# Kernel tuning notes

Measured on AMD Instinct MI355X. Metric: run time of the kernel, lower is better.

The kernel has to match this reference:

```python
import jax, jax.numpy as jnp
import numpy as np

ALPHA = 0.2          # LeakyReLU negative slope
NEG_BIG = -9e15      # mask value from the original code


def setup_inputs() -> dict:
    key = jax.random.key(0)
    k1, k2, k3, k4, k5 = jax.random.split(key, 5)
    N, Fin, Fout, C = 8192, 2048, 256, 8
    x = jax.random.normal(k1, (N, Fin), dtype=jnp.float32)
    # xavier_uniform-ish scale for params
    W = jax.random.normal(k2, (C, Fin, Fout), dtype=jnp.float32) / np.sqrt(Fin).astype(np.float32)
    a = jax.random.normal(k3, (2 * Fout, 1), dtype=jnp.float32) / np.sqrt(2 * Fout).astype(np.float32)
    cam_ids = jax.random.randint(k4, (N,), 0, C, dtype=jnp.int32)
    adj = jax.random.randint(k5, (N, N), 0, 2, dtype=jnp.int32)
    return {"x": x, "W": W, "a": a, "cam_ids": cam_ids, "adj": adj}


def reference(x, W, a, cam_ids, adj):
    N = x.shape[0]
    Fout = W.shape[-1]
    # per-node camera-specific projection: h[i] = x[i] @ W[cam_ids[i]]
    # compute all-camera projections (N, C, Fout) then gather per node;
    # avoids materializing W[cam_ids] of shape (N, Fin, Fout)
    hs = jnp.einsum('nd,cdo->nco', x, W)                       # (N, C, Fout)
    h = jnp.take_along_axis(hs, cam_ids[:, None, None], axis=1)[:, 0, :]  # (N, Fout)
    # e_ij = leakyrelu([h_i, h_j] @ a) = leakyrelu(h_i.a1 + h_j.a2)
    a1 = a[:Fout, 0]
    a2 = a[Fout:, 0]
    e = jax.nn.leaky_relu((h @ a1)[:, None] + (h @ a2)[None, :], ALPHA)  # (N, N)
    att = jnp.where(adj > 0, e, jnp.float32(NEG_BIG))
    att = jax.nn.softmax(att, axis=1)
    # dropout is identity at eval (p applied only in training)
    h_prime = att @ h                                          # (N, Fout)
    return jax.nn.elu(h_prime)                                 # concat=True -> ELU
```

## Files before the change

### kernel.cpp

```cpp
#include <hip/hip_runtime.h>

#define NR 8192
#define FIN 2048
#define FOUT 256
#define ALPHA 0.2f
#define NTMAX 136
#define KS 4
#define KLEN 512
#define NSTEPS 16
#define JC 4
#define NJ 2048

typedef float f32x4 __attribute__((ext_vector_type(4)));
typedef float f32x16 __attribute__((ext_vector_type(16)));
typedef int i32x4 __attribute__((ext_vector_type(4)));
typedef unsigned int u32x4 __attribute__((ext_vector_type(4)));
typedef unsigned short u16x4 __attribute__((ext_vector_type(4)));
typedef unsigned short u16x8 __attribute__((ext_vector_type(8)));
typedef __bf16 bf16x8 __attribute__((ext_vector_type(8)));
typedef _Float16 f16x8 __attribute__((ext_vector_type(8)));

__device__ __forceinline__ unsigned short f2bf(float f){
  unsigned u = __float_as_uint(f);
  return (unsigned short)((u + 0x7fffu + ((u >> 16) & 1u)) >> 16);
}
__device__ __forceinline__ float bf2f(unsigned short b){
  return __uint_as_float(((unsigned)b) << 16);
}
__device__ __forceinline__ void gload16(const void* gptr, void* lptr){
  __builtin_amdgcn_global_load_lds(
      (const __attribute__((address_space(1))) unsigned int*)gptr,
      (__attribute__((address_space(3))) unsigned int*)lptr, 16, 0, 0);
}

#define FBAR() do{ \
  asm volatile("s_waitcnt lgkmcnt(0)" ::: "memory"); \
  __builtin_amdgcn_s_barrier(); \
  __builtin_amdgcn_sched_barrier(0); }while(0)

__global__ __launch_bounds__(256) void k_pre(const float* __restrict__ W,
    _Float16* __restrict__ WhT, const int* __restrict__ cam,
    int* __restrict__ prows, int* __restrict__ tileCam){
  __shared__ __align__(16) char smem[9216];
  int blk = blockIdx.x, t = threadIdx.x;
  if (blk < 1024){
    _Float16 (*tl)[72] = (_Float16(*)[72])smem;
    int k0 = (blk & 31) << 6;
    int n0 = ((blk >> 5) & 3) << 6;
    int c = blk >> 7;
    {
      int kk = t >> 2, nq = (t & 3)*16;
      const float* src = W + ((size_t)c*FIN + k0 + kk)*FOUT + n0 + nq;
      #pragma unroll
      for (int q = 0; q < 4; q++){
        f32x4 v = *(const f32x4*)(src + q*4);
        #pragma unroll
        for (int e = 0; e < 4; e++) tl[nq + q*4 + e][kk] = (_Float16)v[e];
      }
    }
    __syncthreads();
    {
      int nn = t >> 2, kq = (t & 3)*16;
      union { u32x4 v[2]; _Float16 s[16]; } buf;
      #pragma unroll
      for (int e = 0; e < 16; e++) buf.s[e] = tl[nn][kq + e];
      u32x4* dst = (u32x4*)(WhT + ((size_t)c*FOUT + n0 + nn)*FIN + k0 + kq);
      dst[0] = buf.v[0]; dst[1] = buf.v[1];
    }
  } else {
    int (*cnt)[8] = (int(*)[8])smem;
    int* scnt = (int*)(smem + 8192);
    int* tst  = (int*)(smem + 8224);
    int loc[8];
    #pragma unroll
    for (int c = 0; c < 8; c++) loc[c] = 0;
    for (int k = 0; k < 32; k++) loc[cam[t*32 + k] & 7]++;
    #pragma unroll
    for (int c = 0; c < 8; c++) cnt[t][c] = loc[c];
    __syncthreads();
    if (t < 8){
      int s = 0;
      for (int i = 0; i < 256; i++){ int v = cnt[i][t]; cnt[i][t] = s; s += v; }
      scnt[t] = s;
    }
    __syncthreads();
    if (t == 0){
      int ts = 0;
      for (int c = 0; c < 8; c++){ tst[c] = ts; ts += (scnt[c] + 63) >> 6; }
      tst[8] = ts;
    }
    __syncthreads();
    for (int s = t; s < NTMAX*64; s += 256) prows[s] = -1;
    if (t < NTMAX){
      int tc = -1, te = tst[8];
      if (t < te){
        #pragma unroll
        for (int c = 0; c < 8; c++)
          if (t >= tst[c] && t < tst[c+1]) tc = c;
      }
      tileCam[t] = tc;
    }
    __syncthreads();
    int off[8];
    #pragma unroll
    for (int c = 0; c < 8; c++) off[c] = cnt[t][c];
    for (int k = 0; k < 32; k++){
      int n = t*32 + k; int c = cam[n] & 7;
      int slot = off[c]++;
      prows[(tst[c] + (slot >> 6))*64 + (slot & 63)] = n;
    }
  }
}

__global__ __launch_bounds__(256, 3) void k_gmm(const float* __restrict__ x,
    const _Float16* __restrict__ WhT, const int* __restrict__ tileCam,
    const int* __restrict__ prows, float* __restrict__ partial){
  __shared__ __align__(16) char smem[41728];
  int item = blockIdx.x;
  int tile = item >> 2, ks = item & 3;
  int camc = tileCam[tile];
  if (camc < 0) return;
  _Float16* ab = (_Float16*)smem;
  int* rows  = (int*)(smem + 40960);
  int* growL = (int*)(smem + 41216);
  int t = threadIdx.x;
  if (t < 64){
    int r = prows[tile*64 + t];
    rows[t] = r; growL[t] = (r < 0) ? 0 : r;
  }
  __syncthreads();
  int lane = t & 63, w = t >> 6;
  int k0 = ks * KLEN;
  int wr = w >> 1, wc = w & 1;
  int rA = ((t >> 6) & 1)*32 + (t & 31);
  int koffA = (t >> 7)*16 + ((t >> 5) & 1)*8;
  const float* srcA = x + (size_t)growL[rA]*FIN + k0 + koffA;
  const _Float16* srcB[4];
  #pragma unroll
  for (int q = 0; q < 4; q++){
    int c2 = q*256 + t;
    int colg = ((c2 >> 6) & 7)*32 + (t & 31);
    srcB[q] = WhT + ((size_t)camc*FOUT + colg)*FIN + k0
            + (c2 >> 9)*16 + ((t >> 5) & 1)*8;
  }
  f32x16 acc[4];
  #pragma unroll
  for (int nb = 0; nb < 4; nb++)
    #pragma unroll
    for (int r = 0; r < 16; r++) acc[nb][r] = 0.f;
  int cur = 0;
  {
    f32x4 a0 = *(const f32x4*)srcA;
    f32x4 a1 = *(const f32x4*)(srcA + 4);
    #pragma unroll
    for (int q = 0; q < 4; q++) gload16(srcB[q], &ab[2048 + (q*256 + t)*8]);
    f16x8 hv;
    #pragma unroll
    for (int e = 0; e < 4; e++){ hv[e] = (_Float16)a0[e]; hv[4+e] = (_Float16)a1[e]; }
    *(f16x8*)&ab[t*8] = hv;
  }
  __syncthreads();
  for (int s = 0; s < NSTEPS; s++){
    bool have = (s + 1 < NSTEPS);
    int adv = have ? (s + 1)*32 : 0;
    f32x4 na0 = *(const f32x4*)(srcA + adv);
    f32x4 na1 = *(const f32x4*)(srcA + adv + 4);
    if (have){
      #pragma unroll
      for (int q = 0; q < 4; q++)
        gload16(srcB[q] + adv, &ab[(cur ^ 1)*10240 + 2048 + (q*256 + t)*8]);
    }
    const _Float16* base = ab + cur*10240;
    f16x8 af[2]; f16x8 bfr[2][4];
    #pragma unroll
    for (int kk = 0; kk < 2; kk++){
      af[kk] = *(const f16x8*)(base + ((kk*2 + wr)*64 + lane)*8);
      #pragma unroll
      for (int nb = 0; nb < 4; nb++)
        bfr[kk][nb] = *(const f16x8*)(base + 2048 + ((kk*8 + wc*4 + nb)*64 + lane)*8);
    }
    #pragma unroll
    for (int kk = 0; kk < 2; kk++)
      #pragma unroll
      for (int nb = 0; nb < 4; nb++)
        acc[nb] = __builtin_amdgcn_mfma_f32_32x32x16_f16(af[kk], bfr[kk][nb], acc[nb], 0, 0, 0);
    if (have){
      f16x8 hv;
      #pragma unroll
      for (int e = 0; e < 4; e++){ hv[e] = (_Float16)na0[e]; hv[4+e] = (_Float16)na1[e]; }
      *(f16x8*)&ab[(cur ^ 1)*10240 + t*8] = hv;
    }
    __syncthreads();
    cur ^= 1;
  }
  int colb = wc*128;
  #pragma unroll
  for (int nb = 0; nb < 4; nb++){
    #pragma unroll
    for (int r = 0; r < 16; r++){
      int rowl = wr*32 + (r & 3) + 8*(r >> 2) + 4*(lane >> 5);
      int grow = rows[rowl];
      if (grow >= 0)
        partial[((size_t)ks*NR + grow)*FOUT + colb + nb*32 + (lane & 31)] = acc[nb][r];
    }
  }
}

__global__ __launch_bounds__(256) void k_hsumT(const float* __restrict__ partial,
    const float* __restrict__ a, float* __restrict__ s1, float* __restrict__ s2,
    float* __restrict__ bm, unsigned short* __restrict__ hT){
  __shared__ __align__(16) char smem[36096];
  unsigned short* sums = (unsigned short*)smem;
  float* a1l = (float*)(smem + 33792);
  float* a2l = (float*)(smem + 34816);
  float* redv = (float*)(smem + 35840);
  int blk = blockIdx.x, t = threadIdx.x;
  int w = t >> 6, lane = t & 63;
  int r0 = blk*64;
  a1l[t] = a[t]; a2l[t] = a[FOUT + t];
  __syncthreads();
  float bmax = -3.0e38f;
  #pragma unroll
  for (int rep = 0; rep < 16; rep++){
    int row = rep*4 + w;
    const float* pp = partial + (size_t)(r0 + row)*FOUT + lane*4;
    f32x4 s; s[0] = s[1] = s[2] = s[3] = 0.f;
    #pragma unroll
    for (int ks = 0; ks < KS; ks++)
      s += *(const f32x4*)(pp + (size_t)ks*NR*FOUT);
    u16x4 pk;
    #pragma unroll
    for (int e = 0; e < 4; e++) pk[e] = f2bf(s[e]);
    *(u16x4*)&sums[row*264 + lane*4] = pk;
    f32x4 a1v = *(const f32x4*)&a1l[lane*4];
    f32x4 a2v = *(const f32x4*)&a2l[lane*4];
    float p1 = 0.f, p2 = 0.f;
    #pragma unroll
    for (int e = 0; e < 4; e++){ p1 = fmaf(s[e], a1v[e], p1); p2 = fmaf(s[e], a2v[e], p2); }
    #pragma unroll
    for (int off2 = 32; off2 > 0; off2 >>= 1){
      p1 += __shfl_xor(p1, off2);
      p2 += __shfl_xor(p2, off2);
    }
    if (lane == 0){
      s1[r0 + row] = p1; s2[r0 + row] = p2;
      bmax = fmaxf(bmax, p2);
    }
  }
  if (lane == 0) redv[w] = bmax;
  __syncthreads();
  if (t == 0)
    bm[blk] = fmaxf(fmaxf(redv[0], redv[1]), fmaxf(redv[2], redv[3]));
  int c = t;
  #pragma unroll
  for (int q = 0; q < 8; q++){
    u16x8 v;
    #pragma unroll
    for (int e = 0; e < 8; e++) v[e] = sums[(q*8 + e)*264 + c];
    *(u16x8*)(hT + (size_t)c*NR + r0 + q*8) = v;
  }
}

__global__ __launch_bounds__(512, 4) void k_flash(const int* __restrict__ adj,
    const float* __restrict__ s1g, const float* __restrict__ s2g,
    const float* __restrict__ bm, const unsigned short* __restrict__ hT,
    float* __restrict__ hp, float* __restrict__ Dp){
  __shared__ __align__(16) unsigned short hTl[256*64];
  __shared__ __align__(16) unsigned short pl[64][72];
  __shared__ float s1l[64], ml[64], Dl[64], red[8];
  int blk = blockIdx.x, t = threadIdx.x;
  int w = t >> 6, lane = t & 63;
  int it = blk & 127, jc = blk >> 7;
  int i0 = it*64;
  int jbase = jc * NJ;
  {
    float v = (t < 128) ? bm[t] : -3.0e38f;
    #pragma unroll
    for (int off = 32; off > 0; off >>= 1) v = fmaxf(v, __shfl_xor(v, off));
    if (lane == 0) red[w] = v;
  }
  __syncthreads();
  if (t == 0){
    float v = red[0];
    #pragma unroll
    for (int k = 1; k < 8; k++) v = fmaxf(v, red[k]);
    red[0] = v;
  }
  __syncthreads();
  float maxS2 = red[0];
  if (t < 64){
    float sv = s1g[i0 + t];
    s1l[t] = sv;
    float mm = sv + maxS2;
    ml[t] = fmaxf(mm, ALPHA*mm);
  }
  __syncthreads();
  int il = t >> 3, tj = t & 7;
  float s1i = s1l[il], mi = ml[il];
  float Dacc = 0.f;
  f32x16 acc0, acc1;
  #pragma unroll
  for (int k = 0; k < 16; k++){ acc0[k] = 0.f; acc1[k] = 0.f; }
  const unsigned short* hsrc[4];
  int ldst[4];
  #pragma unroll
  for (int q = 0; q < 4; q++){
    int g = t + 512*q;
    int row = g >> 3, part = g & 7;
    hsrc[q] = hT + (size_t)row*NR + jbase + part*8;
    ldst[q] = row*64 + ((part ^ (row & 7))*8);
  }
  const int* arow = adj + (size_t)(i0 + il)*NR + jbase + tj*8;
  i32x4 adx[2][2];
  f32x4 s2x[2][2];
  #pragma unroll
  for (int sl = 0; sl < 2; sl++){
    adx[sl][0] = __builtin_nontemporal_load((const i32x4*)(arow + sl*64));
    adx[sl][1] = __builtin_nontemporal_load((const i32x4*)(arow + sl*64) + 1);
    s2x[sl][0] = *(const f32x4*)(s2g + jbase + sl*64 + tj*8);
    s2x[sl][1] = *(const f32x4*)(s2g + jbase + sl*64 + tj*8 + 4);
  }
  u32x4 hch[4];
  #pragma unroll
  for (int q = 0; q < 4; q++) hch[q] = *(const u32x4*)hsrc[q];
  for (int jt = 0; jt < NJ; jt += 128){
    #pragma unroll
    for (int half = 0; half < 2; half++){
      int jcur = jt + half*64;
      i32x4 c0 = adx[half][0], c1 = adx[half][1];
      f32x4 t0 = s2x[half][0], t1 = s2x[half][1];
      int jn2 = (jcur + 128 < NJ) ? jcur + 128 : 0;
      adx[half][0] = __builtin_nontemporal_load((const i32x4*)(arow + jn2));
      adx[half][1] = __builtin_nontemporal_load((const i32x4*)(arow + jn2) + 1);
      s2x[half][0] = *(const f32x4*)(s2g + jbase + jn2 + tj*8);
      s2x[half][1] = *(const f32x4*)(s2g + jbase + jn2 + tj*8 + 4);
      u16x8 pu;
      float Dloc = 0.f;
      #pragma unroll
      for (int e = 0; e < 4; e++){
        float e0 = s1i + t0[e]; e0 = fmaxf(e0, ALPHA*e0);
        float p0 = (c0[e] > 0) ? __expf(e0 - mi) : 0.f;
        unsigned short b0 = f2bf(p0); pu[e] = b0; Dloc += bf2f(b0);
        float e1 = s1i + t1[e]; e1 = fmaxf(e1, ALPHA*e1);
        float p1 = (c1[e] > 0) ? __expf(e1 - mi) : 0.f;
        unsigned short b1 = f2bf(p1); pu[e + 4] = b1; Dloc += bf2f(b1);
      }
      Dacc += Dloc;
      *(u16x8*)&pl[il][tj*8] = pu;
      #pragma unroll
      for (int q = 0; q < 4; q++) *(u32x4*)&hTl[ldst[q]] = hch[q];
      FBAR();
      int jn1 = (jcur + 64 < NJ) ? jcur + 64 : 0;
      #pragma unroll
      for (int q = 0; q < 4; q++) hch[q] = *(const u32x4*)(hsrc[q] + jn1);
      int nrow = w*32 + (lane & 31);
      #pragma unroll
      for (int ks = 0; ks < 4; ks++){
        int p = ks*2 + (lane >> 5);
        bf16x8 B = *(const bf16x8*)&hTl[nrow*64 + ((p ^ (nrow & 7))*8)];
        int koff = ks*16 + (lane >> 5)*8;
        bf16x8 a0 = *(const bf16x8*)&pl[lane & 31][koff];
        acc0 = __builtin_amdgcn_mfma_f32_32x32x16_bf16(a0, B, acc0, 0, 0, 0);
        bf16x8 a1 = *(const bf16x8*)&pl[32 + (lane & 31)][koff];
        acc1 = __builtin_amdgcn_mfma_f32_32x32x16_bf16(a1, B, acc1, 0, 0, 0);
      }
      FBAR();
    }
  }
  Dacc += __shfl_xor(Dacc, 1);
  Dacc += __shfl_xor(Dacc, 2);
  Dacc += __shfl_xor(Dacc, 4);
  if (tj == 0) Dl[il] = Dacc;
  __syncthreads();
  if (t < 64) Dp[(size_t)jc*NR + i0 + t] = Dl[t];
  float* hpb = hp + (size_t)jc*NR*FOUT;
  int col = w*32 + (lane & 31);
  #pragma unroll
  for (int r = 0; r < 16; r++){
    int rowl = (r & 3) + 8*(r >> 2) + 4*(lane >> 5);
    hpb[(size_t)(i0 + rowl)*FOUT + col] = acc0[r];
    hpb[(size_t)(i0 + 32 + rowl)*FOUT + col] = acc1[r];
  }
}

__global__ __launch_bounds__(256) void k_final(const float* __restrict__ hp,
    const float* __restrict__ Dp, float* __restrict__ out){
  int g = blockIdx.x*256 + threadIdx.x;
  int i = g >> 6, cg4 = (g & 63)*4;
  f32x4 s; s[0] = s[1] = s[2] = s[3] = 0.f;
  float D = 0.f;
  #pragma unroll
  for (int jc = 0; jc < JC; jc++){
    s += *(const f32x4*)(hp + ((size_t)jc*NR + i)*FOUT + cg4);
    D += Dp[(size_t)jc*NR + i];
  }
  float inv = (D > 0.f) ? 1.f / D : 0.f;
  f32x4 o;
  #pragma unroll
  for (int e = 0; e < 4; e++){
    float v = s[e]*inv;
    o[e] = (v > 0.f) ? v : expm1f(v);
  }
  *(f32x4*)(out + (size_t)i*FOUT + cg4) = o;
}

extern "C" void kernel_launch(void* const* d_in, const int* in_sizes, int n_in,
                              void* d_out, int out_size, void* d_ws, size_t ws_size,
                              hipStream_t stream){
  (void)in_sizes; (void)n_in; (void)out_size; (void)ws_size;
  const float* x   = (const float*)d_in[0];
  const float* W   = (const float*)d_in[1];
  const float* a   = (const float*)d_in[2];
  const int*   cam = (const int*)d_in[3];
  const int*   adj = (const int*)d_in[4];
  float* out = (float*)d_out;
  char* ws = (char*)d_ws;

  size_t off = 0;
  auto alloc = [&](size_t b) -> void* {
    void* p = ws + off; off = (off + b + 255) & ~(size_t)255; return p;
  };
  int* tileCam  = (int*)alloc((size_t)NTMAX*4);
  int* prows    = (int*)alloc((size_t)NTMAX*64*4);
  _Float16* WhT = (_Float16*)alloc((size_t)8*FIN*FOUT*2);
  unsigned short* hT = (unsigned short*)alloc((size_t)NR*FOUT*2);
  float* s1 = (float*)alloc((size_t)NR*4);
  float* s2 = (float*)alloc((size_t)NR*4);
  float* bm = (float*)alloc(128*4);
  float* Dp = (float*)alloc((size_t)JC*NR*4);
  float* partial = (float*)alloc((size_t)KS*NR*FOUT*4);
  float* hp = partial;

  hipLaunchKernelGGL(k_pre, dim3(1025), dim3(256), 0, stream,
                     W, WhT, cam, prows, tileCam);
  hipLaunchKernelGGL(k_gmm, dim3(NTMAX*4), dim3(256), 0, stream,
                     x, WhT, tileCam, prows, partial);
  hipLaunchKernelGGL(k_hsumT, dim3(128), dim3(256), 0, stream,
                     partial, a, s1, s2, bm, hT);
  hipLaunchKernelGGL(k_flash, dim3(512), dim3(512), 0, stream,
                     adj, s1, s2, bm, hT, hp, Dp);
  hipLaunchKernelGGL(k_final, dim3((NR*FOUT/4)/256), dim3(256), 0, stream,
                     hp, Dp, out);
}
```

Baseline: 207.3 us.

## Fuse final normalize+ELU into flash kernel via last-block atomic counter

Removes the separate k_final launch. The last of the JC column-chunk blocks for each row tile, detected with an atomic counter, reduces the partial hp/Dp, normalizes and applies ELU directly. It also replaces the custom FBAR barrier (explicit lgkmcnt wait plus sched_barrier) with plain __syncthreads. This saves a launch and some tail latency, but adds fences and atomics and may lose the scheduling control FBAR gave.

```diff
diff --git a/kernel.cpp b/kernel.cpp
--- a/kernel.cpp
+++ b/kernel.cpp
@@ -33,14 +33,10 @@
       (__attribute__((address_space(3))) unsigned int*)lptr, 16, 0, 0);
 }
 
-#define FBAR() do{ \
-  asm volatile("s_waitcnt lgkmcnt(0)" ::: "memory"); \
-  __builtin_amdgcn_s_barrier(); \
-  __builtin_amdgcn_sched_barrier(0); }while(0)
-
 __global__ __launch_bounds__(256) void k_pre(const float* __restrict__ W,
     _Float16* __restrict__ WhT, const int* __restrict__ cam,
-    int* __restrict__ prows, int* __restrict__ tileCam){
+    int* __restrict__ prows, int* __restrict__ tileCam,
+    int* __restrict__ fcnt){
   __shared__ __align__(16) char smem[9216];
   int blk = blockIdx.x, t = threadIdx.x;
   if (blk < 1024){
@@ -68,6 +64,7 @@
       dst[0] = buf.v[0]; dst[1] = buf.v[1];
     }
   } else {
+    if (t < 128) fcnt[t] = 0;
     int (*cnt)[8] = (int(*)[8])smem;
     int* scnt = (int*)(smem + 8192);
     int* tst  = (int*)(smem + 8224);
@@ -264,10 +261,12 @@
 __global__ __launch_bounds__(512, 4) void k_flash(const int* __restrict__ adj,
     const float* __restrict__ s1g, const float* __restrict__ s2g,
     const float* __restrict__ bm, const unsigned short* __restrict__ hT,
-    float* __restrict__ hp, float* __restrict__ Dp){
+    float* __restrict__ hp, float* __restrict__ Dp,
+    int* __restrict__ fcnt, float* __restrict__ outp){
   __shared__ __align__(16) unsigned short hTl[256*64];
   __shared__ __align__(16) unsigned short pl[64][72];
   __shared__ float s1l[64], ml[64], Dl[64], red[8];
+  __shared__ int lastFlag;
   int blk = blockIdx.x, t = threadIdx.x;
   int w = t >> 6, lane = t & 63;
   int it = blk & 127, jc = blk >> 7;
@@ -349,7 +348,7 @@
       *(u16x8*)&pl[il][tj*8] = pu;
       #pragma unroll
       for (int q = 0; q < 4; q++) *(u32x4*)&hTl[ldst[q]] = hch[q];
-      FBAR();
+      __syncthreads();
       int jn1 = (jcur + 64 < NJ) ? jcur + 64 : 0;
       #pragma unroll
       for (int q = 0; q < 4; q++) hch[q] = *(const u32x4*)(hsrc[q] + jn1);
@@ -364,7 +363,7 @@
         bf16x8 a1 = *(const bf16x8*)&pl[32 + (lane & 31)][koff];
         acc1 = __builtin_amdgcn_mfma_f32_32x32x16_bf16(a1, B, acc1, 0, 0, 0);
       }
-      FBAR();
+      __syncthreads();
     }
   }
   Dacc += __shfl_xor(Dacc, 1);
@@ -381,27 +380,37 @@
     hpb[(size_t)(i0 + rowl)*FOUT + col] = acc0[r];
     hpb[(size_t)(i0 + 32 + rowl)*FOUT + col] = acc1[r];
   }
-}
-
-__global__ __launch_bounds__(256) void k_final(const float* __restrict__ hp,
-    const float* __restrict__ Dp, float* __restrict__ out){
-  int g = blockIdx.x*256 + threadIdx.x;
-  int i = g >> 6, cg4 = (g & 63)*4;
-  f32x4 s; s[0] = s[1] = s[2] = s[3] = 0.f;
-  float D = 0.f;
-  #pragma unroll
-  for (int jc = 0; jc < JC; jc++){
-    s += *(const f32x4*)(hp + ((size_t)jc*NR + i)*FOUT + cg4);
-    D += Dp[(size_t)jc*NR + i];
-  }
-  float inv = (D > 0.f) ? 1.f / D : 0.f;
-  f32x4 o;
-  #pragma unroll
-  for (int e = 0; e < 4; e++){
-    float v = s[e]*inv;
-    o[e] = (v > 0.f) ? v : expm1f(v);
-  }
-  *(f32x4*)(out + (size_t)i*FOUT + cg4) = o;
+  __threadfence();
+  __syncthreads();
+  if (t == 0){
+    int done = atomicAdd(&fcnt[it], 1);
+    lastFlag = (done == JC - 1);
+  }
+  __syncthreads();
+  if (lastFlag){
+    __threadfence();
+    #pragma unroll
+    for (int rep = 0; rep < 8; rep++){
+      int u = rep*512 + t;
+      int row = i0 + (u >> 6), cg4 = (u & 63)*4;
+      f32x4 s; s[0] = s[1] = s[2] = s[3] = 0.f;
+      float D = 0.f;
+      #pragma unroll
+      for (int j = 0; j < JC; j++){
+        s += *(const f32x4*)(hp + ((size_t)j*NR + row)*FOUT + cg4);
+        D += Dp[(size_t)j*NR + row];
+      }
+      float inv = (D > 0.f) ? 1.f / D : 0.f;
+      f32x4 o;
+      #pragma unroll
+      for (int e = 0; e < 4; e++){
+        float v = s[e]*inv;
+        o[e] = (v > 0.f) ? v : expm1f(v);
+      }
+      *(f32x4*)(outp + (size_t)row*FOUT + cg4) = o;
+    }
+    if (t == 0) fcnt[it] = 0;
+  }
 }
 
 extern "C" void kernel_launch(void* const* d_in, const int* in_sizes, int n_in,
@@ -422,6 +431,7 @@
   };
   int* tileCam  = (int*)alloc((size_t)NTMAX*4);
   int* prows    = (int*)alloc((size_t)NTMAX*64*4);
+  int* fcnt     = (int*)alloc(128*4);
   _Float16* WhT = (_Float16*)alloc((size_t)8*FIN*FOUT*2);
   unsigned short* hT = (unsigned short*)alloc((size_t)NR*FOUT*2);
   float* s1 = (float*)alloc((size_t)NR*4);
@@ -432,13 +442,11 @@
   float* hp = partial;
 
   hipLaunchKernelGGL(k_pre, dim3(1025), dim3(256), 0, stream,
-                     W, WhT, cam, prows, tileCam);
+                     W, WhT, cam, prows, tileCam, fcnt);
   hipLaunchKernelGGL(k_gmm, dim3(NTMAX*4), dim3(256), 0, stream,
                      x, WhT, tileCam, prows, partial);
   hipLaunchKernelGGL(k_hsumT, dim3(128), dim3(256), 0, stream,
                      partial, a, s1, s2, bm, hT);
   hipLaunchKernelGGL(k_flash, dim3(512), dim3(512), 0, stream,
-                     adj, s1, s2, bm, hT, hp, Dp);
-  hipLaunchKernelGGL(k_final, dim3((NR*FOUT/4)/256), dim3(256), 0, stream,
-                     hp, Dp, out);
-}
+                     adj, s1, s2, bm, hT, hp, Dp, fcnt, out);
+}
```

Result: slower. 405.7 us (+95.8%).
